# Optimization experiments

Measured on AMD Instinct MI355X. Metric: run time of the kernel, lower is better.

## Reference

```python
import jax, jax.numpy as jnp
import numpy as np
from jax import lax

B, C, H, W = 4, 256, 64, 64
C8 = C // 8  # 32


def setup_inputs() -> dict:
    key = jax.random.key(0)
    ks = jax.random.split(key, 8)
    x = jax.random.normal(ks[0], (B, C, H, W), jnp.float32)
    # 1x1 conv weights stored as [out_ch, in_ch]
    wb = jax.random.normal(ks[1], (C8, 2 * C), jnp.float32) * 0.02
    bb = jax.random.normal(ks[2], (C8,), jnp.float32) * 0.02
    wc = jax.random.normal(ks[3], (C8, 2 * C), jnp.float32) * 0.02
    bc = jax.random.normal(ks[4], (C8,), jnp.float32) * 0.02
    wd = jax.random.normal(ks[5], (C, 2 * C), jnp.float32) * 0.02
    bd = jax.random.normal(ks[6], (C,), jnp.float32) * 0.02
    alpha = jnp.float32(0.5)  # nn.Parameter(zeros(1)) at init; nonzero for a meaningful test
    return {"x": x, "wb": wb, "bb": bb, "wc": wc, "bc": bc, "wd": wd, "bd": bd, "alpha": alpha}


def reference(x, wb, bb, wc, bc, wd, bd, alpha):
    b, c, h, w = x.shape
    n = h * w
    pad = [(0, 0), (0, 0), (1, 1), (1, 1)]
    # F.avg_pool2d(k=3, s=1, p=1) with count_include_pad=True -> window-sum / 9
    x_avg = lax.reduce_window(x, 0.0, lax.add, (1, 1, 3, 3), (1, 1, 1, 1), pad) / 9.0
    x_max = lax.reduce_window(x, -jnp.inf, lax.max, (1, 1, 3, 3), (1, 1, 1, 1), pad)
    cat = jnp.concatenate([x_avg, x_max], axis=1)  # [B, 2C, H, W]
    catf = cat.reshape(b, 2 * c, n)                # [B, 2C, N]
    # 1x1 convs == per-pixel linear projections
    feat_b = jnp.einsum('oc,bcn->bon', wb, catf) + bb[None, :, None]  # [B, C8, N]
    feat_c = jnp.einsum('oc,bcn->bon', wc, catf) + bc[None, :, None]  # [B, C8, N]
    feat_d = jnp.einsum('oc,bcn->bon', wd, catf) + bd[None, :, None]  # [B, C,  N]
    # attention_s = softmax(feat_b^T @ feat_c) over last dim -> [B, N, N]
    attn = jax.nn.softmax(jnp.einsum('bon,bom->bnm', feat_b, feat_c), axis=-1)
    # feat_e = feat_d @ attn^T -> [B, C, N]
    feat_e = jnp.einsum('bcn,bmn->bcm', feat_d, attn).reshape(b, c, h, w)
    return alpha * feat_e + (1.0 - alpha) * x
```

## Files before the change

kernel.cpp:

```cpp
#include <hip/hip_runtime.h>
#include <hip/hip_bf16.h>

typedef __hip_bfloat16 bf16;
typedef __attribute__((ext_vector_type(8))) short s8v;
typedef __attribute__((ext_vector_type(4))) float f4v;

__device__ __forceinline__ ushort f2u(float f) {
    bf16 h = __float2bfloat16(f);
    return *(ushort*)&h;
}


__global__ __launch_bounds__(64) void wcvt_kernel(
    const float* __restrict__ wb, const float* __restrict__ wc,
    const float* __restrict__ wd, ushort* __restrict__ Wf) {
    int ot = blockIdx.x;
    int kc = blockIdx.y;
    int l = threadIdx.x;
    int o = ot * 16 + (l & 15);
    int k0 = kc * 32 + (l >> 4) * 8;
    const float* wr = (o < 32) ? wb + (size_t)o * 512
                    : (o < 64) ? wc + (size_t)(o - 32) * 512
                               : wd + (size_t)(o - 64) * 512;
    float4 f0 = *(const float4*)(wr + k0);
    float4 f1 = *(const float4*)(wr + k0 + 4);
    ushort tmp[8] = {f2u(f0.x), f2u(f0.y), f2u(f0.z), f2u(f0.w),
                     f2u(f1.x), f2u(f1.y), f2u(f1.z), f2u(f1.w)};
    *(uint4*)(Wf + kc * 10240 + ot * 512 + l * 8) = *(uint4*)tmp;
}

__global__ __launch_bounds__(256) void pool_kernel(const float* __restrict__ x,
                                                   ushort* __restrict__ cat) {
    __shared__ float Xs[3][64][66];
    int tid = threadIdx.x;
    int bid = blockIdx.x;
    int b = bid >> 8, h = (bid >> 2) & 63, cg = bid & 3;
    bool hasU = (h > 0), hasD = (h < 63);
    #pragma unroll
    for (int pp = 0; pp < 12; ++pp) {
        int linear = pp * 256 + tid;
        int w4 = linear & 15;
        int cs = (linear >> 4) & 63;
        int dh = linear >> 10;
        int hh = h + dh - 1;
        float4 f = {0.f, 0.f, 0.f, 0.f};
        if ((unsigned)hh < 64u)
            f = *(const float4*)(x + ((size_t)(b * 256 + cg * 64 + cs)) * 4096
                                 + hh * 64 + w4 * 4);
        Xs[dh][w4 * 4 + 0][cs] = f.x;
        Xs[dh][w4 * 4 + 1][cs] = f.y;
        Xs[dh][w4 * 4 + 2][cs] = f.z;
        Xs[dh][w4 * 4 + 3][cs] = f.w;
    }
    __syncthreads();
    int cs = tid & 63, ws = tid >> 6;
    float vs[18], vm[18];
    #pragma unroll
    for (int j = 0; j < 18; ++j) {
        int w = ws * 16 - 1 + j;
        if ((unsigned)w < 64u) {
            float u = Xs[0][w][cs], m = Xs[1][w][cs], d = Xs[2][w][cs];
            vs[j] = u + m + d;
            float mx = m;
            if (hasU) mx = fmaxf(mx, u);
            if (hasD) mx = fmaxf(mx, d);
            vm[j] = mx;
        } else { vs[j] = 0.f; vm[j] = -3.4e38f; }
    }
    size_t nb = ((size_t)b * 4096 + h * 64 + ws * 16) * 512 + cg * 64 + cs;
    #pragma unroll
    for (int i = 0; i < 16; ++i) {
        float sum = vs[i] + vs[i + 1] + vs[i + 2];
        float mx  = fmaxf(fmaxf(vm[i], vm[i + 1]), vm[i + 2]);
        cat[nb + (size_t)i * 512]       = f2u(sum * (1.f / 9.f));
        cat[nb + (size_t)i * 512 + 256] = f2u(mx);
    }
}

__global__ __launch_bounds__(256, 2) void proj_kernel(
    const ushort* __restrict__ cat, const ushort* __restrict__ Wf,
    const float* __restrict__ bb, const float* __restrict__ bc,
    const float* __restrict__ bd,
    ushort* __restrict__ Qb, ushort* __restrict__ Kb, ushort* __restrict__ Vf) {
    __shared__ __align__(16) ushort As[32][72];
    __shared__ __align__(16) ushort Vls[256][40];
    int tid = threadIdx.x;
    int l = tid & 63, w = tid >> 6;
    int lm = l & 15, q = l >> 4;
    int n0 = blockIdx.x * 32;
    f4v acc[2][5];
    #pragma unroll
    for (int mt = 0; mt < 2; ++mt)
        #pragma unroll
        for (int ot = 0; ot < 5; ++ot)
            #pragma unroll
            for (int i = 0; i < 4; ++i) acc[mt][ot][i] = 0.f;

    const ushort* wfb = Wf + (w * 5) * 512 + l * 8;
    int sr = tid >> 3, sko = (tid & 7) * 8;
    const ushort* srow = cat + (size_t)(n0 + sr) * 512 + sko;

    for (int kc = 0; kc < 8; ++kc) {
        *(uint4*)&As[sr][sko] = *(const uint4*)(srow + kc * 64);
        __syncthreads();
        #pragma unroll
        for (int ks = 0; ks < 2; ++ks) {
            int kci = kc * 2 + ks;
            s8v bf[5];
            #pragma unroll
            for (int ot = 0; ot < 5; ++ot)
                bf[ot] = *(const s8v*)(wfb + kci * 10240 + ot * 512);
            s8v a0 = *(const s8v*)&As[lm][ks * 32 + q * 8];
            s8v a1 = *(const s8v*)&As[16 + lm][ks * 32 + q * 8];
            #pragma unroll
            for (int ot = 0; ot < 5; ++ot) {
                acc[0][ot] = __builtin_amdgcn_mfma_f32_16x16x32_bf16(a0, bf[ot], acc[0][ot], 0, 0, 0);
                acc[1][ot] = __builtin_amdgcn_mfma_f32_16x16x32_bf16(a1, bf[ot], acc[1][ot], 0, 0, 0);
            }
        }
        __syncthreads();
    }
    #pragma unroll
    for (int ot = 0; ot < 5; ++ot) {
        int o = w * 80 + ot * 16 + lm;
        if (o < 32) {
            float bias = bb[o];
            #pragma unroll
            for (int mt = 0; mt < 2; ++mt)
                #pragma unroll
                for (int r = 0; r < 4; ++r)
                    Qb[(size_t)(n0 + mt * 16 + q * 4 + r) * 32 + o]
                        = f2u(acc[mt][ot][r] + bias);
        } else if (o < 64) {
            float bias = bc[o - 32];
            #pragma unroll
            for (int mt = 0; mt < 2; ++mt)
                #pragma unroll
                for (int r = 0; r < 4; ++r)
                    Kb[(size_t)(n0 + mt * 16 + q * 4 + r) * 32 + (o - 32)]
                        = f2u(acc[mt][ot][r] + bias);
        } else {
            int c = o - 64;
            float bias = bd[c];
            #pragma unroll
            for (int mt = 0; mt < 2; ++mt) {
                ushort tmp[4];
                #pragma unroll
                for (int r = 0; r < 4; ++r) tmp[r] = f2u(acc[mt][ot][r] + bias);
                *(uint2*)&Vls[c][mt * 16 + q * 4] = *(uint2*)tmp;
            }
        }
    }
    __syncthreads();
    {
        int bidx = n0 >> 12;
        size_t fb = ((size_t)bidx << 20) + (size_t)((n0 & 4095) >> 5) * 8192 + l * 8;
        #pragma unroll
        for (int i = 0; i < 4; ++i) {
            int cb = w * 4 + i;
            *(uint4*)(Vf + fb + cb * 512) = *(const uint4*)&Vls[cb * 16 + lm][q * 8];
        }
    }
}

__global__ __launch_bounds__(512, 2) void attn_kernel(
    const ushort* __restrict__ Qb, const ushort* __restrict__ Kb,
    const ushort* __restrict__ Vf, const float* __restrict__ x,
    const float* __restrict__ alphap, float* __restrict__ out) {
    __shared__ __align__(16) ushort Ps[2][64][72];
    __shared__ float Obuf[4][64][17];
    __shared__ float Lpart[4][64];
    __shared__ float Lrow[64];
    int tid = threadIdx.x;
    int l = tid & 63, w = tid >> 6;
    int lm = l & 15, q = l >> 4;
    int nsw = w & 3, kh = w >> 2;
    int bid = blockIdx.x;
    int xcd = bid & 7;
    int b = xcd & 3;
    int midx = (bid >> 3) + ((xcd >> 2) << 5);
    int m0 = midx << 6;
    size_t bN = (size_t)b << 12;

    s8v Qf[2];
    {
        const ushort* qb = Qb + (bN + m0 + kh * 32) * 32;
        Qf[0] = *(const s8v*)(qb + (size_t)(lm) * 32 + q * 8);
        Qf[1] = *(const s8v*)(qb + (size_t)(16 + lm) * 32 + q * 8);
    }
    const ushort* kbp = Kb + (bN + nsw * 16 + lm) * 32 + q * 8;
    const ushort* vfp = Vf + ((size_t)b << 20) + kh * 8192 + (nsw * 4) * 512 + l * 8;

    f4v acc[4][4];
    #pragma unroll
    for (int mt = 0; mt < 4; ++mt)
        #pragma unroll
        for (int ct = 0; ct < 4; ++ct)
            #pragma unroll
            for (int i = 0; i < 4; ++i) acc[mt][ct][i] = 0.f;
    float La0 = 0.f, La1 = 0.f;

    s8v kfA, kfB, vfA[4], vfB[4];
    kfA = *(const s8v*)kbp;
    #pragma unroll
    for (int ct = 0; ct < 4; ++ct) vfA[ct] = *(const s8v*)(vfp + ct * 512);

#define TILE_BODY(TT, KF, VF, KFN, VFN, DOPF)                                     \
    {                                                                             \
        int p = (TT) & 1;                                                         \
        f4v S0 = {0.f, 0.f, 0.f, 0.f}, S1 = {0.f, 0.f, 0.f, 0.f};                 \
        S0 = __builtin_amdgcn_mfma_f32_16x16x32_bf16(KF, Qf[0], S0, 0, 0, 0);     \
        S1 = __builtin_amdgcn_mfma_f32_16x16x32_bf16(KF, Qf[1], S1, 0, 0, 0);     \
        ushort e0[4], e1[4];                                                      \
        _Pragma("unroll")                                                         \
        for (int r = 0; r < 4; ++r) {                                             \
            float f0 = __expf(fminf(S0[r], 60.f));                                \
            float f1 = __expf(fminf(S1[r], 60.f));                                \
            La0 += f0; La1 += f1;                                                 \
            e0[r] = f2u(f0); e1[r] = f2u(f1);                                     \
        }                                                                         \
        *(uint2*)&Ps[p][kh * 32 + lm][nsw * 16 + q * 4]      = *(uint2*)e0;       \
        *(uint2*)&Ps[p][kh * 32 + 16 + lm][nsw * 16 + q * 4] = *(uint2*)e1;       \
        __syncthreads();                                                          \
        if (DOPF) {                                                               \
            KFN = *(const s8v*)(kbp + (size_t)((TT) + 1) * 2048);                 \
            const ushort* vn = vfp + (size_t)((TT) + 1) * 16384;                  \
            _Pragma("unroll")                                                     \
            for (int ct = 0; ct < 4; ++ct)                                        \
                VFN[ct] = *(const s8v*)(vn + ct * 512);                           \
        }                                                                         \
        s8v Af0 = *(const s8v*)&Ps[p][lm][kh * 32 + q * 8];                       \
        s8v Af1 = *(const s8v*)&Ps[p][16 + lm][kh * 32 + q * 8];                  \
        s8v Af2 = *(const s8v*)&Ps[p][32 + lm][kh * 32 + q * 8];                  \
        s8v Af3 = *(const s8v*)&Ps[p][48 + lm][kh * 32 + q * 8];                  \
        _Pragma("unroll")                                                         \
        for (int ct = 0; ct < 4; ++ct) {                                          \
            acc[0][ct] = __builtin_amdgcn_mfma_f32_16x16x32_bf16(Af0, VF[ct], acc[0][ct], 0, 0, 0); \
            acc[1][ct] = __builtin_amdgcn_mfma_f32_16x16x32_bf16(Af1, VF[ct], acc[1][ct], 0, 0, 0); \
            acc[2][ct] = __builtin_amdgcn_mfma_f32_16x16x32_bf16(Af2, VF[ct], acc[2][ct], 0, 0, 0); \
            acc[3][ct] = __builtin_amdgcn_mfma_f32_16x16x32_bf16(Af3, VF[ct], acc[3][ct], 0, 0, 0); \
        }                                                                         \
    }

    for (int t = 0; t < 64; t += 2) {
        TILE_BODY(t,     kfA, vfA, kfB, vfB, true);
        TILE_BODY(t + 1, kfB, vfB, kfA, vfA, (t + 2) < 64);
    }
#undef TILE_BODY

    La0 += __shfl_xor(La0, 16, 64); La0 += __shfl_xor(La0, 32, 64);
    La1 += __shfl_xor(La1, 16, 64); La1 += __shfl_xor(La1, 32, 64);
    if (q == 0) {
        Lpart[nsw][kh * 32 + lm]      = La0;
        Lpart[nsw][kh * 32 + 16 + lm] = La1;
    }
    __syncthreads();
    if (tid < 64)
        Lrow[tid] = Lpart[0][tid] + Lpart[1][tid] + Lpart[2][tid] + Lpart[3][tid];
    __syncthreads();
    #pragma unroll
    for (int ct = 0; ct < 4; ++ct) {
        if (kh == 1) {
            #pragma unroll
            for (int mt = 0; mt < 4; ++mt)
                #pragma unroll
                for (int r = 0; r < 4; ++r)
                    Obuf[nsw][mt * 16 + q * 4 + r][lm] = acc[mt][ct][r];
        }
        __syncthreads();
        if (kh == 0) {
            #pragma unroll
            for (int mt = 0; mt < 4; ++mt)
                #pragma unroll
                for (int r = 0; r < 4; ++r)
                    acc[mt][ct][r] += Obuf[nsw][mt * 16 + q * 4 + r][lm];
        }
        __syncthreads();
    }
    if (kh == 0) {
        float alpha = alphap[0];
        float ra = 1.f - alpha;
        #pragma unroll
        for (int mt = 0; mt < 4; ++mt) {
            float L0 = Lrow[mt * 16 + q * 4 + 0];
            float L1 = Lrow[mt * 16 + q * 4 + 1];
            float L2 = Lrow[mt * 16 + q * 4 + 2];
            float L3 = Lrow[mt * 16 + q * 4 + 3];
            #pragma unroll
            for (int ct = 0; ct < 4; ++ct) {
                int cc = nsw * 64 + ct * 16 + lm;
                size_t base = ((size_t)(b * 256 + cc)) * 4096 + m0 + mt * 16 + q * 4;
                float4 xv = *(const float4*)(x + base);
                float4 ov;
                ov.x = alpha * (acc[mt][ct][0] / L0) + ra * xv.x;
                ov.y = alpha * (acc[mt][ct][1] / L1) + ra * xv.y;
                ov.z = alpha * (acc[mt][ct][2] / L2) + ra * xv.z;
                ov.w = alpha * (acc[mt][ct][3] / L3) + ra * xv.w;
                *(float4*)(out + base) = ov;
            }
        }
    }
}

extern "C" void kernel_launch(void* const* d_in, const int* in_sizes, int n_in,
                              void* d_out, int out_size, void* d_ws, size_t ws_size,
                              hipStream_t stream) {
    const float* x  = (const float*)d_in[0];
    const float* wb = (const float*)d_in[1];
    const float* bb = (const float*)d_in[2];
    const float* wc = (const float*)d_in[3];
    const float* bc = (const float*)d_in[4];
    const float* wd = (const float*)d_in[5];
    const float* bd = (const float*)d_in[6];
    const float* al = (const float*)d_in[7];
    float* out = (float*)d_out;

    char* ws = (char*)d_ws;
    ushort* cat = (ushort*)ws;
    ushort* Qb  = (ushort*)(ws + 16777216);
    ushort* Kb  = (ushort*)(ws + 17825792);
    ushort* Vf  = (ushort*)(ws + 18874368);
    ushort* Wf  = (ushort*)(ws + 27262976);

    wcvt_kernel<<<dim3(20, 16), dim3(64), 0, stream>>>(wb, wc, wd, Wf);
    pool_kernel<<<dim3(1024), dim3(256), 0, stream>>>(x, cat);
    proj_kernel<<<dim3(512), dim3(256), 0, stream>>>(cat, Wf, bb, bc, bd,
                                                     Qb, Kb, Vf);
    attn_kernel<<<dim3(256), dim3(512), 0, stream>>>(Qb, Kb, Vf, x, al, out);
}
```

Before: 171.8 us.

## Software-pipeline attention QK/exp one tile ahead and fold weight conversion into pool kernel

The attention loop is restructured so the score MFMA and exponentials for tile t+1 are computed and written into the other P buffer while the PV MFMAs for tile t run. A single barrier now sits at the end of each iteration, and K fragments are prefetched two tiles ahead. Separately, the weight bf16 conversion kernel is merged into the pool kernel as 80 extra blocks, removing one launch. This adds register pressure from holding two K fragments and two V fragment sets.

```diff
diff --git a/kernel.cpp b/kernel.cpp
--- a/kernel.cpp
+++ b/kernel.cpp
@@ -11,29 +11,29 @@
 }
 
 
-__global__ __launch_bounds__(64) void wcvt_kernel(
+__global__ __launch_bounds__(256) void pool_kernel(
+    const float* __restrict__ x, ushort* __restrict__ cat,
     const float* __restrict__ wb, const float* __restrict__ wc,
     const float* __restrict__ wd, ushort* __restrict__ Wf) {
-    int ot = blockIdx.x;
-    int kc = blockIdx.y;
-    int l = threadIdx.x;
-    int o = ot * 16 + (l & 15);
-    int k0 = kc * 32 + (l >> 4) * 8;
-    const float* wr = (o < 32) ? wb + (size_t)o * 512
-                    : (o < 64) ? wc + (size_t)(o - 32) * 512
-                               : wd + (size_t)(o - 64) * 512;
-    float4 f0 = *(const float4*)(wr + k0);
-    float4 f1 = *(const float4*)(wr + k0 + 4);
-    ushort tmp[8] = {f2u(f0.x), f2u(f0.y), f2u(f0.z), f2u(f0.w),
-                     f2u(f1.x), f2u(f1.y), f2u(f1.z), f2u(f1.w)};
-    *(uint4*)(Wf + kc * 10240 + ot * 512 + l * 8) = *(uint4*)tmp;
-}
-
-__global__ __launch_bounds__(256) void pool_kernel(const float* __restrict__ x,
-                                                   ushort* __restrict__ cat) {
+    int bid = blockIdx.x;
+    int tid = threadIdx.x;
+    if (bid >= 1024) {
+        int f = (bid - 1024) * 4 + (tid >> 6);
+        int l = tid & 63;
+        int ot = f % 20, kc = f / 20;
+        int o = ot * 16 + (l & 15);
+        int k0 = kc * 32 + (l >> 4) * 8;
+        const float* wr = (o < 32) ? wb + (size_t)o * 512
+                        : (o < 64) ? wc + (size_t)(o - 32) * 512
+                                   : wd + (size_t)(o - 64) * 512;
+        float4 f0 = *(const float4*)(wr + k0);
+        float4 f1 = *(const float4*)(wr + k0 + 4);
+        ushort tmp[8] = {f2u(f0.x), f2u(f0.y), f2u(f0.z), f2u(f0.w),
+                         f2u(f1.x), f2u(f1.y), f2u(f1.z), f2u(f1.w)};
+        *(uint4*)(Wf + kc * 10240 + ot * 512 + l * 8) = *(uint4*)tmp;
+        return;
+    }
     __shared__ float Xs[3][64][66];
-    int tid = threadIdx.x;
-    int bid = blockIdx.x;
     int b = bid >> 8, h = (bid >> 2) & 63, cg = bid & 3;
     bool hasU = (h > 0), hasD = (h < 63);
     #pragma unroll
@@ -200,34 +200,52 @@
             for (int i = 0; i < 4; ++i) acc[mt][ct][i] = 0.f;
     float La0 = 0.f, La1 = 0.f;
 
-    s8v kfA, kfB, vfA[4], vfB[4];
-    kfA = *(const s8v*)kbp;
+    s8v kf0 = *(const s8v*)kbp;
+    s8v kf1 = *(const s8v*)(kbp + 2048);
+    s8v vfA[4], vfB[4];
     #pragma unroll
     for (int ct = 0; ct < 4; ++ct) vfA[ct] = *(const s8v*)(vfp + ct * 512);
-
-#define TILE_BODY(TT, KF, VF, KFN, VFN, DOPF)                                     \
+    {
+        f4v S0 = {0.f, 0.f, 0.f, 0.f}, S1 = {0.f, 0.f, 0.f, 0.f};
+        S0 = __builtin_amdgcn_mfma_f32_16x16x32_bf16(kf0, Qf[0], S0, 0, 0, 0);
+        S1 = __builtin_amdgcn_mfma_f32_16x16x32_bf16(kf0, Qf[1], S1, 0, 0, 0);
+        ushort e0[4], e1[4];
+        #pragma unroll
+        for (int r = 0; r < 4; ++r) {
+            float f0 = __expf(fminf(S0[r], 60.f));
+            float f1 = __expf(fminf(S1[r], 60.f));
+            La0 += f0; La1 += f1;
+            e0[r] = f2u(f0); e1[r] = f2u(f1);
+        }
+        *(uint2*)&Ps[0][kh * 32 + lm][nsw * 16 + q * 4]      = *(uint2*)e0;
+        *(uint2*)&Ps[0][kh * 32 + 16 + lm][nsw * 16 + q * 4] = *(uint2*)e1;
+    }
+    __syncthreads();
+
+#define TILE_BODY(TT, KFS, KFP, VCUR, VNXT)                                       \
     {                                                                             \
         int p = (TT) & 1;                                                         \
-        f4v S0 = {0.f, 0.f, 0.f, 0.f}, S1 = {0.f, 0.f, 0.f, 0.f};                 \
-        S0 = __builtin_amdgcn_mfma_f32_16x16x32_bf16(KF, Qf[0], S0, 0, 0, 0);     \
-        S1 = __builtin_amdgcn_mfma_f32_16x16x32_bf16(KF, Qf[1], S1, 0, 0, 0);     \
-        ushort e0[4], e1[4];                                                      \
-        _Pragma("unroll")                                                         \
-        for (int r = 0; r < 4; ++r) {                                             \
-            float f0 = __expf(fminf(S0[r], 60.f));                                \
-            float f1 = __expf(fminf(S1[r], 60.f));                                \
-            La0 += f0; La1 += f1;                                                 \
-            e0[r] = f2u(f0); e1[r] = f2u(f1);                                     \
+        if ((TT) < 63) {                                                          \
+            f4v S0 = {0.f, 0.f, 0.f, 0.f}, S1 = {0.f, 0.f, 0.f, 0.f};             \
+            S0 = __builtin_amdgcn_mfma_f32_16x16x32_bf16(KFS, Qf[0], S0, 0, 0, 0);\
+            S1 = __builtin_amdgcn_mfma_f32_16x16x32_bf16(KFS, Qf[1], S1, 0, 0, 0);\
+            ushort e0[4], e1[4];                                                  \
+            _Pragma("unroll")                                                     \
+            for (int r = 0; r < 4; ++r) {                                         \
+                float f0 = __expf(fminf(S0[r], 60.f));                            \
+                float f1 = __expf(fminf(S1[r], 60.f));                            \
+                La0 += f0; La1 += f1;                                             \
+                e0[r] = f2u(f0); e1[r] = f2u(f1);                                 \
+            }                                                                     \
+            *(uint2*)&Ps[1 - p][kh * 32 + lm][nsw * 16 + q * 4]      = *(uint2*)e0;\
+            *(uint2*)&Ps[1 - p][kh * 32 + 16 + lm][nsw * 16 + q * 4] = *(uint2*)e1;\
         }                                                                         \
-        *(uint2*)&Ps[p][kh * 32 + lm][nsw * 16 + q * 4]      = *(uint2*)e0;       \
-        *(uint2*)&Ps[p][kh * 32 + 16 + lm][nsw * 16 + q * 4] = *(uint2*)e1;       \
-        __syncthreads();                                                          \
-        if (DOPF) {                                                               \
-            KFN = *(const s8v*)(kbp + (size_t)((TT) + 1) * 2048);                 \
+        if ((TT) < 62) KFP = *(const s8v*)(kbp + (size_t)((TT) + 2) * 2048);      \
+        if ((TT) < 63) {                                                          \
             const ushort* vn = vfp + (size_t)((TT) + 1) * 16384;                  \
             _Pragma("unroll")                                                     \
             for (int ct = 0; ct < 4; ++ct)                                        \
-                VFN[ct] = *(const s8v*)(vn + ct * 512);                           \
+                VNXT[ct] = *(const s8v*)(vn + ct * 512);                          \
         }                                                                         \
         s8v Af0 = *(const s8v*)&Ps[p][lm][kh * 32 + q * 8];                       \
         s8v Af1 = *(const s8v*)&Ps[p][16 + lm][kh * 32 + q * 8];                  \
@@ -235,16 +253,17 @@
         s8v Af3 = *(const s8v*)&Ps[p][48 + lm][kh * 32 + q * 8];                  \
         _Pragma("unroll")                                                         \
         for (int ct = 0; ct < 4; ++ct) {                                          \
-            acc[0][ct] = __builtin_amdgcn_mfma_f32_16x16x32_bf16(Af0, VF[ct], acc[0][ct], 0, 0, 0); \
-            acc[1][ct] = __builtin_amdgcn_mfma_f32_16x16x32_bf16(Af1, VF[ct], acc[1][ct], 0, 0, 0); \
-            acc[2][ct] = __builtin_amdgcn_mfma_f32_16x16x32_bf16(Af2, VF[ct], acc[2][ct], 0, 0, 0); \
-            acc[3][ct] = __builtin_amdgcn_mfma_f32_16x16x32_bf16(Af3, VF[ct], acc[3][ct], 0, 0, 0); \
+            acc[0][ct] = __builtin_amdgcn_mfma_f32_16x16x32_bf16(Af0, VCUR[ct], acc[0][ct], 0, 0, 0); \
+            acc[1][ct] = __builtin_amdgcn_mfma_f32_16x16x32_bf16(Af1, VCUR[ct], acc[1][ct], 0, 0, 0); \
+            acc[2][ct] = __builtin_amdgcn_mfma_f32_16x16x32_bf16(Af2, VCUR[ct], acc[2][ct], 0, 0, 0); \
+            acc[3][ct] = __builtin_amdgcn_mfma_f32_16x16x32_bf16(Af3, VCUR[ct], acc[3][ct], 0, 0, 0); \
         }                                                                         \
+        __syncthreads();                                                          \
     }
 
     for (int t = 0; t < 64; t += 2) {
-        TILE_BODY(t,     kfA, vfA, kfB, vfB, true);
-        TILE_BODY(t + 1, kfB, vfB, kfA, vfA, (t + 2) < 64);
+        TILE_BODY(t,     kf1, kf0, vfA, vfB);
+        TILE_BODY(t + 1, kf0, kf1, vfB, vfA);
     }
 #undef TILE_BODY
 
@@ -322,8 +341,7 @@
     ushort* Vf  = (ushort*)(ws + 18874368);
     ushort* Wf  = (ushort*)(ws + 27262976);
 
-    wcvt_kernel<<<dim3(20, 16), dim3(64), 0, stream>>>(wb, wc, wd, Wf);
-    pool_kernel<<<dim3(1024), dim3(256), 0, stream>>>(x, cat);
+    pool_kernel<<<dim3(1104), dim3(256), 0, stream>>>(x, cat, wb, wc, wd, Wf);
     proj_kernel<<<dim3(512), dim3(256), 0, stream>>>(cat, Wf, bb, bc, bd,
                                                      Qb, Kb, Vf);
     attn_kernel<<<dim3(256), dim3(512), 0, stream>>>(Qb, Kb, Vf, x, al, out);
```

Measured after the change: 164.1 us. 1.05x faster.
